# Kernel tuning notes

Hardware: AMD Instinct MI355X
Metric: run time of the kernel (lower is better)

The kernel has to match this reference:

```python
import jax, jax.numpy as jnp
import numpy as np

H = 512  # hidden_size


def setup_inputs() -> dict:
    key = jax.random.key(0)
    k1, k2, k3, k4, k5 = jax.random.split(key, 5)
    B, S = 32, 2048
    hidden = jax.random.normal(k1, (1, B, H), dtype=jnp.float32)
    encoder_outputs = jax.random.normal(k2, (B, S, 2 * H), dtype=jnp.float32)
    # nn.Linear(3H, H): weight [H, 3H], store transposed [3H, H] for x @ W
    scale_a = 1.0 / np.sqrt(3 * H)
    Wa = jax.random.uniform(k3, (3 * H, H), jnp.float32, -scale_a, scale_a)
    ba = jax.random.uniform(k4, (H,), jnp.float32, -scale_a, scale_a)
    # nn.Linear(H, 1, bias=False): weight [1, H] -> store as [H]
    scale_v = 1.0 / np.sqrt(H)
    v = jax.random.uniform(k5, (H,), jnp.float32, -scale_v, scale_v)
    return {"hidden": hidden, "encoder_outputs": encoder_outputs,
            "Wa": Wa, "ba": ba, "v": v}


def reference(hidden, encoder_outputs, Wa, ba, v):
    # hidden: [1, B, H] -> [B, H]; encoder_outputs: [B, S, 2H]
    h = jnp.squeeze(hidden, axis=0)                      # [B, H]
    # Split concat-linear into two projections (same math as cat + matmul):
    Wh, We = Wa[:H], Wa[H:]                              # [H, H], [2H, H]
    # energy: [B, S, H] = tanh(h Wh + enc We + b), h broadcast over S
    energy = jnp.tanh(h @ Wh + jnp.einsum('bse,eh->bsh', encoder_outputs, We)[..., :, :] + ba) if False else \
             jnp.tanh((h @ Wh)[:, None, :] + jnp.einsum('bse,eh->bsh', encoder_outputs, We) + ba)
    scores = jnp.einsum('bsh,h->bs', energy, v)          # [B, S]
    attention_weights = jax.nn.softmax(scores, axis=1)   # [B, S]
    context = jnp.einsum('bs,bse->be', attention_weights, encoder_outputs)  # [B, 2H]
    return context, attention_weights
```

## Files before the change

kernel.cpp:

```cpp
#include <hip/hip_runtime.h>

typedef unsigned short ushort_t;
typedef __attribute__((ext_vector_type(8))) short bf16x8;
typedef __attribute__((ext_vector_type(4))) float f32x4;

#define H 512
#define E 1024
#define S 2048
#define B 32

__device__ __forceinline__ ushort_t f2bf(float f) {
    unsigned u = __float_as_uint(f);
    unsigned r = (u + 0x7FFFu + ((u >> 16) & 1u)) >> 16;
    return (ushort_t)r;
}

__global__ void prep_hb(const float* __restrict__ hidden, const float* __restrict__ Wa,
                        const float* __restrict__ ba, float* __restrict__ hb) {
    int b = blockIdx.x, tid = threadIdx.x;
    __shared__ float hs[H];
    hs[tid]       = hidden[b * H + tid];
    hs[tid + 256] = hidden[b * H + tid + 256];
    __syncthreads();
    float a0 = 0.f, a1 = 0.f;
    for (int k = 0; k < H; ++k) {
        float hv = hs[k];
        a0 += hv * Wa[(size_t)k * H + tid];
        a1 += hv * Wa[(size_t)k * H + tid + 256];
    }
    hb[b * H + tid]       = a0 + ba[tid];
    hb[b * H + tid + 256] = a1 + ba[tid + 256];
}

__global__ void prep_wef(const float* __restrict__ Wa, ushort_t* __restrict__ wef) {
    int g = blockIdx.x * 256 + threadIdx.x;
    int kt = g >> 11, nt = (g >> 6) & 31, l = g & 63;
    int kbase = kt * 32 + ((l >> 4) << 3);
    int n = nt * 16 + (l & 15);
    #pragma unroll
    for (int j = 0; j < 8; ++j)
        wef[(size_t)g * 8 + j] = f2bf(Wa[(size_t)(H + kbase + j) * H + n]);
}

__launch_bounds__(256, 2)
__global__ void score_kernel(const float* __restrict__ enc, const ushort_t* __restrict__ wef,
                             const float* __restrict__ hb, const float* __restrict__ v,
                             float* __restrict__ scores) {
    int b = blockIdx.y;
    int s0 = blockIdx.x * 64;
    int tid = threadIdx.x;
    int wave = tid >> 6, lane = tid & 63;
    int q = lane >> 4, nl = lane & 15;

    __shared__ ushort_t As[64 * 72];
    __shared__ float sred[4][64];

    f32x4 acc[4][8] = {};

    const float* Arow = enc + ((size_t)b * S + s0) * E;
    int srow = tid >> 3;
    int scol = (tid & 7) * 8;

    for (int kb = 0; kb < 16; ++kb) {
        #pragma unroll
        for (int it = 0; it < 2; ++it) {
            int r = srow + it * 32;
            const float* src = Arow + (size_t)r * E + kb * 64 + scol;
            float4 x = *(const float4*)src;
            float4 y = *(const float4*)(src + 4);
            uint4 u;
            u.x = (unsigned)f2bf(x.x) | ((unsigned)f2bf(x.y) << 16);
            u.y = (unsigned)f2bf(x.z) | ((unsigned)f2bf(x.w) << 16);
            u.z = (unsigned)f2bf(y.x) | ((unsigned)f2bf(y.y) << 16);
            u.w = (unsigned)f2bf(y.z) | ((unsigned)f2bf(y.w) << 16);
            *(uint4*)&As[r * 72 + scol] = u;
        }
        __syncthreads();
        #pragma unroll
        for (int ks = 0; ks < 2; ++ks) {
            int kt = kb * 2 + ks;
            bf16x8 afr[4];
            #pragma unroll
            for (int mt = 0; mt < 4; ++mt) {
                int m = mt * 16 + nl;
                afr[mt] = *(const bf16x8*)&As[m * 72 + ks * 32 + q * 8];
            }
            #pragma unroll
            for (int ntl = 0; ntl < 8; ++ntl) {
                int nt = wave * 8 + ntl;
                bf16x8 bfr = *(const bf16x8*)&wef[((size_t)(kt * 32 + nt) * 64 + lane) * 8];
                #pragma unroll
                for (int mt = 0; mt < 4; ++mt)
                    acc[mt][ntl] = __builtin_amdgcn_mfma_f32_16x16x32_bf16(
                        afr[mt], bfr, acc[mt][ntl], 0, 0, 0);
            }
        }
        __syncthreads();
    }

    float p[16];
    #pragma unroll
    for (int i = 0; i < 16; ++i) p[i] = 0.f;
    #pragma unroll
    for (int ntl = 0; ntl < 8; ++ntl) {
        int n = wave * 128 + ntl * 16 + nl;
        float hv = hb[b * H + n];
        float vv = v[n];
        #pragma unroll
        for (int mt = 0; mt < 4; ++mt)
            #pragma unroll
            for (int r = 0; r < 4; ++r)
                p[mt * 4 + r] += vv * tanhf(acc[mt][ntl][r] + hv);
    }
    #pragma unroll
    for (int off = 1; off < 16; off <<= 1) {
        #pragma unroll
        for (int i = 0; i < 16; ++i) p[i] += __shfl_xor(p[i], off, 64);
    }
    if (nl == 0) {
        #pragma unroll
        for (int mt = 0; mt < 4; ++mt)
            #pragma unroll
            for (int r = 0; r < 4; ++r)
                sred[wave][mt * 16 + q * 4 + r] = p[mt * 4 + r];
    }
    __syncthreads();
    if (tid < 64) {
        float s = sred[0][tid] + sred[1][tid] + sred[2][tid] + sred[3][tid];
        scores[(size_t)b * S + s0 + tid] = s;
    }
}

__global__ void softmax_kernel(const float* __restrict__ scores, float* __restrict__ out) {
    int b = blockIdx.x, tid = threadIdx.x;
    const float* row = scores + (size_t)b * S;
    float loc[8];
    float mx = -3.4e38f;
    #pragma unroll
    for (int i = 0; i < 8; ++i) { loc[i] = row[tid + i * 256]; mx = fmaxf(mx, loc[i]); }
    #pragma unroll
    for (int off = 32; off > 0; off >>= 1) mx = fmaxf(mx, __shfl_xor(mx, off, 64));
    __shared__ float wm[4], wsm[4];
    if ((tid & 63) == 0) wm[tid >> 6] = mx;
    __syncthreads();
    mx = fmaxf(fmaxf(wm[0], wm[1]), fmaxf(wm[2], wm[3]));
    float sum = 0.f;
    #pragma unroll
    for (int i = 0; i < 8; ++i) { loc[i] = __expf(loc[i] - mx); sum += loc[i]; }
    #pragma unroll
    for (int off = 32; off > 0; off >>= 1) sum += __shfl_xor(sum, off, 64);
    if ((tid & 63) == 0) wsm[tid >> 6] = sum;
    __syncthreads();
    sum = wsm[0] + wsm[1] + wsm[2] + wsm[3];
    float inv = 1.f / sum;
    #pragma unroll
    for (int i = 0; i < 8; ++i) out[B * E + (size_t)b * S + tid + i * 256] = loc[i] * inv;
    #pragma unroll
    for (int i = 0; i < 4; ++i) out[(size_t)b * E + tid + i * 256] = 0.f;
}

__global__ void context_kernel(const float* __restrict__ enc, const float* __restrict__ w_attn,
                               float* __restrict__ out_ctx) {
    int et = blockIdx.x, sc = blockIdx.y, b = blockIdx.z;
    int e = et * 256 + threadIdx.x;
    const float* w  = w_attn + (size_t)b * S + sc * 256;
    const float* ep = enc + ((size_t)b * S + sc * 256) * E + e;
    float acc = 0.f;
    #pragma unroll 4
    for (int s = 0; s < 256; ++s) acc += w[s] * ep[(size_t)s * E];
    atomicAdd(&out_ctx[(size_t)b * E + e], acc);
}

extern "C" void kernel_launch(void* const* d_in, const int* in_sizes, int n_in,
                              void* d_out, int out_size, void* d_ws, size_t ws_size,
                              hipStream_t stream) {
    const float* hidden = (const float*)d_in[0];
    const float* enc    = (const float*)d_in[1];
    const float* Wa     = (const float*)d_in[2];
    const float* ba     = (const float*)d_in[3];
    const float* v      = (const float*)d_in[4];
    float* out = (float*)d_out;

    char* ws = (char*)d_ws;
    ushort_t* wef = (ushort_t*)ws;
    float* hb     = (float*)(ws + (1 << 20));
    float* scores = (float*)(ws + (1 << 20) + (1 << 16));

    prep_hb<<<B, 256, 0, stream>>>(hidden, Wa, ba, hb);
    prep_wef<<<256, 256, 0, stream>>>(Wa, wef);
    score_kernel<<<dim3(S / 64, B), 256, 0, stream>>>(enc, wef, hb, v, scores);
    softmax_kernel<<<B, 256, 0, stream>>>(scores, out);
    context_kernel<<<dim3(4, 8, B), 256, 0, stream>>>(enc, out + B * E, out);
}
```

Before: 539.4 us.

## Double-buffer score GEMM with async LDS loads, split hb prep and vectorize context

The score kernel now double-buffers both operands. Weight tiles stream into LDS through global_load_lds, and encoder rows are prefetched two k-steps ahead in registers, so global latency overlaps the MFMA work. prep_hb splits the K dimension across 8 blocks per batch and combines the partials with atomics after a memset, which gives more parallelism. The context kernel is reorganised to use float4 loads over 128-row chunks. The costs are more LDS per block, which may reduce occupancy, and extra atomic traffic.

```diff
diff --git a/kernel.cpp b/kernel.cpp
--- a/kernel.cpp
+++ b/kernel.cpp
@@ -15,21 +15,29 @@
     return (ushort_t)r;
 }
 
+__device__ __forceinline__ uint4 pack8(float4 x, float4 y) {
+    uint4 u;
+    u.x = (unsigned)f2bf(x.x) | ((unsigned)f2bf(x.y) << 16);
+    u.y = (unsigned)f2bf(x.z) | ((unsigned)f2bf(x.w) << 16);
+    u.z = (unsigned)f2bf(y.x) | ((unsigned)f2bf(y.y) << 16);
+    u.w = (unsigned)f2bf(y.z) | ((unsigned)f2bf(y.w) << 16);
+    return u;
+}
+
 __global__ void prep_hb(const float* __restrict__ hidden, const float* __restrict__ Wa,
                         const float* __restrict__ ba, float* __restrict__ hb) {
-    int b = blockIdx.x, tid = threadIdx.x;
-    __shared__ float hs[H];
-    hs[tid]       = hidden[b * H + tid];
-    hs[tid + 256] = hidden[b * H + tid + 256];
-    __syncthreads();
+    int b = blockIdx.x, kc = blockIdx.y, tid = threadIdx.x;
+    const float* hp = hidden + b * H + kc * 64;
     float a0 = 0.f, a1 = 0.f;
-    for (int k = 0; k < H; ++k) {
-        float hv = hs[k];
-        a0 += hv * Wa[(size_t)k * H + tid];
-        a1 += hv * Wa[(size_t)k * H + tid + 256];
-    }
-    hb[b * H + tid]       = a0 + ba[tid];
-    hb[b * H + tid + 256] = a1 + ba[tid + 256];
+    #pragma unroll 8
+    for (int k = 0; k < 64; ++k) {
+        float hv = hp[k];
+        a0 += hv * Wa[(size_t)(kc * 64 + k) * H + tid];
+        a1 += hv * Wa[(size_t)(kc * 64 + k) * H + tid + 256];
+    }
+    if (kc == 0) { a0 += ba[tid]; a1 += ba[tid + 256]; }
+    atomicAdd(&hb[b * H + tid], a0);
+    atomicAdd(&hb[b * H + tid + 256], a1);
 }
 
 __global__ void prep_wef(const float* __restrict__ Wa, ushort_t* __restrict__ wef) {
@@ -52,48 +60,65 @@
     int wave = tid >> 6, lane = tid & 63;
     int q = lane >> 4, nl = lane & 15;
 
-    __shared__ ushort_t As[64 * 72];
+    __shared__ ushort_t Bs[2][32 * 64 * 8];
+    __shared__ ushort_t As[2][64 * 40];
     __shared__ float sred[4][64];
 
     f32x4 acc[4][8] = {};
 
-    const float* Arow = enc + ((size_t)b * S + s0) * E;
-    int srow = tid >> 3;
-    int scol = (tid & 7) * 8;
-
-    for (int kb = 0; kb < 16; ++kb) {
-        #pragma unroll
-        for (int it = 0; it < 2; ++it) {
-            int r = srow + it * 32;
-            const float* src = Arow + (size_t)r * E + kb * 64 + scol;
-            float4 x = *(const float4*)src;
-            float4 y = *(const float4*)(src + 4);
-            uint4 u;
-            u.x = (unsigned)f2bf(x.x) | ((unsigned)f2bf(x.y) << 16);
-            u.y = (unsigned)f2bf(x.z) | ((unsigned)f2bf(x.w) << 16);
-            u.z = (unsigned)f2bf(y.x) | ((unsigned)f2bf(y.y) << 16);
-            u.w = (unsigned)f2bf(y.z) | ((unsigned)f2bf(y.w) << 16);
-            *(uint4*)&As[r * 72 + scol] = u;
+    int arow = tid >> 2, acol = (tid & 3) * 8;
+    const float* asrc = enc + ((size_t)b * S + s0 + arow) * E + acol;
+
+    const ushort_t* bsrc = wef + (size_t)wave * 4096 + (size_t)lane * 8;
+
+    float4 areg[2][2];
+    areg[0][0] = *(const float4*)(asrc);
+    areg[0][1] = *(const float4*)(asrc + 4);
+    areg[1][0] = *(const float4*)(asrc + 32);
+    areg[1][1] = *(const float4*)(asrc + 36);
+
+    #pragma unroll
+    for (int j = 0; j < 8; ++j)
+        __builtin_amdgcn_global_load_lds(
+            (const __attribute__((address_space(1))) unsigned*)(bsrc + j * 512),
+            (__attribute__((address_space(3))) unsigned*)(&Bs[0][wave * 4096 + j * 512]),
+            16, 0, 0);
+
+    *(uint4*)&As[0][arow * 40 + acol] = pack8(areg[0][0], areg[0][1]);
+    __syncthreads();
+
+    for (int kt = 0; kt < 32; ++kt) {
+        int cur = kt & 1;
+        ushort_t* Ac = &As[cur][0];
+        ushort_t* Bc = &Bs[cur][0];
+
+        if (kt < 31) {
+            const ushort_t* bs = bsrc + (size_t)(kt + 1) * 16384;
+            #pragma unroll
+            for (int j = 0; j < 8; ++j)
+                __builtin_amdgcn_global_load_lds(
+                    (const __attribute__((address_space(1))) unsigned*)(bs + j * 512),
+                    (__attribute__((address_space(3))) unsigned*)(&Bs[1 - cur][wave * 4096 + j * 512]),
+                    16, 0, 0);
+            *(uint4*)&As[1 - cur][arow * 40 + acol] =
+                pack8(areg[1 - cur][0], areg[1 - cur][1]);
         }
-        __syncthreads();
-        #pragma unroll
-        for (int ks = 0; ks < 2; ++ks) {
-            int kt = kb * 2 + ks;
-            bf16x8 afr[4];
-            #pragma unroll
-            for (int mt = 0; mt < 4; ++mt) {
-                int m = mt * 16 + nl;
-                afr[mt] = *(const bf16x8*)&As[m * 72 + ks * 32 + q * 8];
-            }
-            #pragma unroll
-            for (int ntl = 0; ntl < 8; ++ntl) {
-                int nt = wave * 8 + ntl;
-                bf16x8 bfr = *(const bf16x8*)&wef[((size_t)(kt * 32 + nt) * 64 + lane) * 8];
-                #pragma unroll
-                for (int mt = 0; mt < 4; ++mt)
-                    acc[mt][ntl] = __builtin_amdgcn_mfma_f32_16x16x32_bf16(
-                        afr[mt], bfr, acc[mt][ntl], 0, 0, 0);
-            }
+        if (kt < 30) {
+            areg[cur][0] = *(const float4*)(asrc + (size_t)(kt + 2) * 32);
+            areg[cur][1] = *(const float4*)(asrc + (size_t)(kt + 2) * 32 + 4);
+        }
+
+        bf16x8 afr[4];
+        #pragma unroll
+        for (int mt = 0; mt < 4; ++mt)
+            afr[mt] = *(const bf16x8*)&Ac[(mt * 16 + nl) * 40 + q * 8];
+        #pragma unroll
+        for (int ntl = 0; ntl < 8; ++ntl) {
+            bf16x8 bfr = *(const bf16x8*)&Bc[((wave * 8 + ntl) * 64 + lane) * 8];
+            #pragma unroll
+            for (int mt = 0; mt < 4; ++mt)
+                acc[mt][ntl] = __builtin_amdgcn_mfma_f32_16x16x32_bf16(
+                    afr[mt], bfr, acc[mt][ntl], 0, 0, 0);
         }
         __syncthreads();
     }
@@ -161,14 +186,22 @@
 
 __global__ void context_kernel(const float* __restrict__ enc, const float* __restrict__ w_attn,
                                float* __restrict__ out_ctx) {
-    int et = blockIdx.x, sc = blockIdx.y, b = blockIdx.z;
-    int e = et * 256 + threadIdx.x;
-    const float* w  = w_attn + (size_t)b * S + sc * 256;
-    const float* ep = enc + ((size_t)b * S + sc * 256) * E + e;
-    float acc = 0.f;
+    int sc = blockIdx.x, b = blockIdx.y;
+    int e = threadIdx.x * 4;
+    const float* w  = w_attn + (size_t)b * S + sc * 128;
+    const float* ep = enc + ((size_t)b * S + sc * 128) * E + e;
+    float a0 = 0.f, a1 = 0.f, a2 = 0.f, a3 = 0.f;
     #pragma unroll 4
-    for (int s = 0; s < 256; ++s) acc += w[s] * ep[(size_t)s * E];
-    atomicAdd(&out_ctx[(size_t)b * E + e], acc);
+    for (int s = 0; s < 128; ++s) {
+        float ws = w[s];
+        float4 x = *(const float4*)(ep + (size_t)s * E);
+        a0 += ws * x.x; a1 += ws * x.y; a2 += ws * x.z; a3 += ws * x.w;
+    }
+    float* dst = &out_ctx[(size_t)b * E + e];
+    atomicAdd(dst + 0, a0);
+    atomicAdd(dst + 1, a1);
+    atomicAdd(dst + 2, a2);
+    atomicAdd(dst + 3, a3);
 }
 
 extern "C" void kernel_launch(void* const* d_in, const int* in_sizes, int n_in,
@@ -186,9 +219,10 @@
     float* hb     = (float*)(ws + (1 << 20));
     float* scores = (float*)(ws + (1 << 20) + (1 << 16));
 
-    prep_hb<<<B, 256, 0, stream>>>(hidden, Wa, ba, hb);
+    hipMemsetAsync(hb, 0, B * H * sizeof(float), stream);
+    prep_hb<<<dim3(B, 8), 256, 0, stream>>>(hidden, Wa, ba, hb);
     prep_wef<<<256, 256, 0, stream>>>(Wa, wef);
     score_kernel<<<dim3(S / 64, B), 256, 0, stream>>>(enc, wef, hb, v, scores);
     softmax_kernel<<<B, 256, 0, stream>>>(scores, out);
-    context_kernel<<<dim3(4, 8, B), 256, 0, stream>>>(enc, out + B * E, out);
-}
+    context_kernel<<<dim3(16, B), 256, 0, stream>>>(enc, out + B * E, out);
+}
```

Result: slower. 557.4 us (+3.3%).

## Restructure score GEMM with double-buffered LDS, register prefetch, and larger tiles

Applied to the files above, without the earlier changes.

The score kernel moves to 128-row tiles with 512 threads and stages a full 256-wide K chunk of the encoder in double-buffered shared memory. Global loads for the next chunk and the weight fragments two steps ahead overlap with the MFMA work on the current chunk. The bf16 conversion now uses a cheaper round-and-permute pack, and tanh is computed through exp. prep_hb and context_kernel are also reworked, the latter using float4 loads over 64-row chunks; the larger LDS footprint (about 136KB) may limit occupancy.

```diff
diff --git a/kernel.cpp b/kernel.cpp
--- a/kernel.cpp
+++ b/kernel.cpp
@@ -15,21 +15,36 @@
     return (ushort_t)r;
 }
 
+__device__ __forceinline__ unsigned pkbf(float x, float y) {
+    unsigned u0 = __float_as_uint(x) + 0x8000u;
+    unsigned u1 = __float_as_uint(y) + 0x8000u;
+    return __builtin_amdgcn_perm(u1, u0, 0x07060302u);
+}
+
+__device__ __forceinline__ uint4 pk8(float4 a, float4 b) {
+    uint4 u;
+    u.x = pkbf(a.x, a.y); u.y = pkbf(a.z, a.w);
+    u.z = pkbf(b.x, b.y); u.w = pkbf(b.z, b.w);
+    return u;
+}
+
+__device__ __forceinline__ int boff(int slot) { return (slot << 4) + ((slot >> 4) << 4); }
+
 __global__ void prep_hb(const float* __restrict__ hidden, const float* __restrict__ Wa,
                         const float* __restrict__ ba, float* __restrict__ hb) {
-    int b = blockIdx.x, tid = threadIdx.x;
+    int b = blockIdx.x, n = threadIdx.x;
     __shared__ float hs[H];
-    hs[tid]       = hidden[b * H + tid];
-    hs[tid + 256] = hidden[b * H + tid + 256];
-    __syncthreads();
-    float a0 = 0.f, a1 = 0.f;
-    for (int k = 0; k < H; ++k) {
-        float hv = hs[k];
-        a0 += hv * Wa[(size_t)k * H + tid];
-        a1 += hv * Wa[(size_t)k * H + tid + 256];
-    }
-    hb[b * H + tid]       = a0 + ba[tid];
-    hb[b * H + tid + 256] = a1 + ba[tid + 256];
+    hs[n] = hidden[b * H + n];
+    __syncthreads();
+    float a0 = 0.f, a1 = 0.f, a2 = 0.f, a3 = 0.f;
+    #pragma unroll 4
+    for (int k = 0; k < H; k += 4) {
+        a0 += hs[k]     * Wa[(size_t)k * H + n];
+        a1 += hs[k + 1] * Wa[(size_t)(k + 1) * H + n];
+        a2 += hs[k + 2] * Wa[(size_t)(k + 2) * H + n];
+        a3 += hs[k + 3] * Wa[(size_t)(k + 3) * H + n];
+    }
+    hb[b * H + n] = a0 + a1 + a2 + a3 + ba[n];
 }
 
 __global__ void prep_wef(const float* __restrict__ Wa, ushort_t* __restrict__ wef) {
@@ -42,91 +57,129 @@
         wef[(size_t)g * 8 + j] = f2bf(Wa[(size_t)(H + kbase + j) * H + n]);
 }
 
-__launch_bounds__(256, 2)
+__launch_bounds__(512, 2)
 __global__ void score_kernel(const float* __restrict__ enc, const ushort_t* __restrict__ wef,
                              const float* __restrict__ hb, const float* __restrict__ v,
                              float* __restrict__ scores) {
-    int b = blockIdx.y;
-    int s0 = blockIdx.x * 64;
-    int tid = threadIdx.x;
-    int wave = tid >> 6, lane = tid & 63;
-    int q = lane >> 4, nl = lane & 15;
-
-    __shared__ ushort_t As[64 * 72];
-    __shared__ float sred[4][64];
-
-    f32x4 acc[4][8] = {};
-
-    const float* Arow = enc + ((size_t)b * S + s0) * E;
-    int srow = tid >> 3;
-    int scol = (tid & 7) * 8;
-
-    for (int kb = 0; kb < 16; ++kb) {
-        #pragma unroll
-        for (int it = 0; it < 2; ++it) {
-            int r = srow + it * 32;
-            const float* src = Arow + (size_t)r * E + kb * 64 + scol;
-            float4 x = *(const float4*)src;
-            float4 y = *(const float4*)(src + 4);
-            uint4 u;
-            u.x = (unsigned)f2bf(x.x) | ((unsigned)f2bf(x.y) << 16);
-            u.y = (unsigned)f2bf(x.z) | ((unsigned)f2bf(x.w) << 16);
-            u.z = (unsigned)f2bf(y.x) | ((unsigned)f2bf(y.y) << 16);
-            u.w = (unsigned)f2bf(y.z) | ((unsigned)f2bf(y.w) << 16);
-            *(uint4*)&As[r * 72 + scol] = u;
+    const int tid = threadIdx.x;
+    const int wave = tid >> 6, lane = tid & 63;
+    const int qq = lane >> 4, nl = lane & 15;
+    const int b = blockIdx.y, s0 = blockIdx.x * 128;
+
+    __shared__ char arena[2 * 69632];
+    __shared__ float sred[8 * 128];
+
+    f32x4 acc[8][4] = {};
+
+    const int sr = tid >> 2;
+    const int c2 = tid & 3;
+    const float* ap = enc + ((size_t)b * S + s0 + sr) * E;
+    const int wbase = (sr >> 4) * 64 + (sr & 15) + 16 * c2;
+
+    const ushort_t* wb = wef + (size_t)(wave * 4) * 512 + lane * 8;
+
+    #pragma unroll
+    for (int h = 0; h < 2; ++h) {
+        float4 t0[4], t1[4];
+        #pragma unroll
+        for (int i2 = 0; i2 < 4; ++i2) {
+            const float* s = ap + (size_t)((h * 4 + i2) * 4 + c2) * 8;
+            t0[i2] = *(const float4*)s;
+            t1[i2] = *(const float4*)(s + 4);
+        }
+        #pragma unroll
+        for (int i2 = 0; i2 < 4; ++i2) {
+            int i = h * 4 + i2;
+            *(uint4*)(arena + boff(i * 512 + wbase)) = pk8(t0[i2], t1[i2]);
+        }
+    }
+
+    bf16x8 bq[2][4];
+    #pragma unroll
+    for (int ntl = 0; ntl < 4; ++ntl) {
+        bq[0][ntl] = *(const bf16x8*)(wb + ntl * 512);
+        bq[1][ntl] = *(const bf16x8*)(wb + 16384 + ntl * 512);
+    }
+    __syncthreads();
+
+    float4 ua[2][2];
+    int buf = 0;
+    for (int q4 = 0; q4 < 4; ++q4) {
+        char* cb = arena + buf * 69632;
+        char* nb = arena + (buf ^ 1) * 69632;
+        #pragma unroll
+        for (int j = 0; j < 8; ++j) {
+            const int kt = q4 * 8 + j;
+            bf16x8 bc[4];
+            #pragma unroll
+            for (int ntl = 0; ntl < 4; ++ntl) bc[ntl] = bq[kt & 1][ntl];
+            if (kt < 30) {
+                #pragma unroll
+                for (int ntl = 0; ntl < 4; ++ntl)
+                    bq[kt & 1][ntl] =
+                        *(const bf16x8*)(wb + (size_t)(kt + 2) * 16384 + ntl * 512);
+            }
+            if (q4 < 3) {
+                if (j >= 2)
+                    *(uint4*)(nb + boff((j - 2) * 512 + wbase)) =
+                        pk8(ua[j & 1][0], ua[j & 1][1]);
+                const float* sld = ap + (q4 + 1) * 256 + (size_t)(j * 4 + c2) * 8;
+                ua[j & 1][0] = *(const float4*)sld;
+                ua[j & 1][1] = *(const float4*)(sld + 4);
+            }
+            bf16x8 afr[8];
+            #pragma unroll
+            for (int mt = 0; mt < 8; ++mt)
+                afr[mt] = *(const bf16x8*)(cb + boff((j * 8 + mt) * 64 + lane));
+            #pragma unroll
+            for (int ntl = 0; ntl < 4; ++ntl)
+                #pragma unroll
+                for (int mt = 0; mt < 8; ++mt)
+                    acc[mt][ntl] = __builtin_amdgcn_mfma_f32_16x16x32_bf16(
+                        afr[mt], bc[ntl], acc[mt][ntl], 0, 0, 0);
+        }
+        if (q4 < 3) {
+            *(uint4*)(nb + boff(6 * 512 + wbase)) = pk8(ua[0][0], ua[0][1]);
+            *(uint4*)(nb + boff(7 * 512 + wbase)) = pk8(ua[1][0], ua[1][1]);
         }
         __syncthreads();
-        #pragma unroll
-        for (int ks = 0; ks < 2; ++ks) {
-            int kt = kb * 2 + ks;
-            bf16x8 afr[4];
-            #pragma unroll
-            for (int mt = 0; mt < 4; ++mt) {
-                int m = mt * 16 + nl;
-                afr[mt] = *(const bf16x8*)&As[m * 72 + ks * 32 + q * 8];
-            }
-            #pragma unroll
-            for (int ntl = 0; ntl < 8; ++ntl) {
-                int nt = wave * 8 + ntl;
-                bf16x8 bfr = *(const bf16x8*)&wef[((size_t)(kt * 32 + nt) * 64 + lane) * 8];
-                #pragma unroll
-                for (int mt = 0; mt < 4; ++mt)
-                    acc[mt][ntl] = __builtin_amdgcn_mfma_f32_16x16x32_bf16(
-                        afr[mt], bfr, acc[mt][ntl], 0, 0, 0);
-            }
-        }
-        __syncthreads();
-    }
-
-    float p[16];
-    #pragma unroll
-    for (int i = 0; i < 16; ++i) p[i] = 0.f;
-    #pragma unroll
-    for (int ntl = 0; ntl < 8; ++ntl) {
-        int n = wave * 128 + ntl * 16 + nl;
+        buf ^= 1;
+    }
+
+    float p[32];
+    #pragma unroll
+    for (int i = 0; i < 32; ++i) p[i] = 0.f;
+    #pragma unroll
+    for (int ntl = 0; ntl < 4; ++ntl) {
+        int n = wave * 64 + ntl * 16 + nl;
         float hv = hb[b * H + n];
         float vv = v[n];
         #pragma unroll
-        for (int mt = 0; mt < 4; ++mt)
-            #pragma unroll
-            for (int r = 0; r < 4; ++r)
-                p[mt * 4 + r] += vv * tanhf(acc[mt][ntl][r] + hv);
+        for (int mt = 0; mt < 8; ++mt)
+            #pragma unroll
+            for (int rr = 0; rr < 4; ++rr) {
+                float x = acc[mt][ntl][rr] + hv;
+                float t = __expf(2.f * x);
+                p[mt * 4 + rr] += vv * ((t - 1.f) / (t + 1.f));
+            }
     }
     #pragma unroll
     for (int off = 1; off < 16; off <<= 1) {
         #pragma unroll
-        for (int i = 0; i < 16; ++i) p[i] += __shfl_xor(p[i], off, 64);
+        for (int i = 0; i < 32; ++i) p[i] += __shfl_xor(p[i], off, 64);
     }
     if (nl == 0) {
         #pragma unroll
-        for (int mt = 0; mt < 4; ++mt)
-            #pragma unroll
-            for (int r = 0; r < 4; ++r)
-                sred[wave][mt * 16 + q * 4 + r] = p[mt * 4 + r];
-    }
-    __syncthreads();
-    if (tid < 64) {
-        float s = sred[0][tid] + sred[1][tid] + sred[2][tid] + sred[3][tid];
+        for (int mt = 0; mt < 8; ++mt)
+            #pragma unroll
+            for (int rr = 0; rr < 4; ++rr)
+                sred[wave * 128 + mt * 16 + qq * 4 + rr] = p[mt * 4 + rr];
+    }
+    __syncthreads();
+    if (tid < 128) {
+        float s = 0.f;
+        #pragma unroll
+        for (int w = 0; w < 8; ++w) s += sred[w * 128 + tid];
         scores[(size_t)b * S + s0 + tid] = s;
     }
 }
@@ -161,14 +214,22 @@
 
 __global__ void context_kernel(const float* __restrict__ enc, const float* __restrict__ w_attn,
                                float* __restrict__ out_ctx) {
-    int et = blockIdx.x, sc = blockIdx.y, b = blockIdx.z;
-    int e = et * 256 + threadIdx.x;
-    const float* w  = w_attn + (size_t)b * S + sc * 256;
-    const float* ep = enc + ((size_t)b * S + sc * 256) * E + e;
-    float acc = 0.f;
-    #pragma unroll 4
-    for (int s = 0; s < 256; ++s) acc += w[s] * ep[(size_t)s * E];
-    atomicAdd(&out_ctx[(size_t)b * E + e], acc);
+    int sc = blockIdx.x, b = blockIdx.y;
+    int e = threadIdx.x * 4;
+    const float* w  = w_attn + (size_t)b * S + sc * 64;
+    const float* ep = enc + ((size_t)b * S + sc * 64) * E + e;
+    float a0 = 0.f, a1 = 0.f, a2 = 0.f, a3 = 0.f;
+    #pragma unroll 16
+    for (int s = 0; s < 64; ++s) {
+        float ws = w[s];
+        float4 x = *(const float4*)(ep + (size_t)s * E);
+        a0 += ws * x.x; a1 += ws * x.y; a2 += ws * x.z; a3 += ws * x.w;
+    }
+    float* dst = &out_ctx[(size_t)b * E + e];
+    atomicAdd(dst + 0, a0);
+    atomicAdd(dst + 1, a1);
+    atomicAdd(dst + 2, a2);
+    atomicAdd(dst + 3, a3);
 }
 
 extern "C" void kernel_launch(void* const* d_in, const int* in_sizes, int n_in,
@@ -186,9 +247,9 @@
     float* hb     = (float*)(ws + (1 << 20));
     float* scores = (float*)(ws + (1 << 20) + (1 << 16));
 
-    prep_hb<<<B, 256, 0, stream>>>(hidden, Wa, ba, hb);
+    prep_hb<<<B, 512, 0, stream>>>(hidden, Wa, ba, hb);
     prep_wef<<<256, 256, 0, stream>>>(Wa, wef);
-    score_kernel<<<dim3(S / 64, B), 256, 0, stream>>>(enc, wef, hb, v, scores);
+    score_kernel<<<dim3(S / 128, B), 512, 0, stream>>>(enc, wef, hb, v, scores);
     softmax_kernel<<<B, 256, 0, stream>>>(scores, out);
-    context_kernel<<<dim3(4, 8, B), 256, 0, stream>>>(enc, out + B * E, out);
-}
+    context_kernel<<<dim3(32, B), 256, 0, stream>>>(enc, out + B * E, out);
+}
```

Result: slower. 576.3 us (+6.8%).
